# Performance work log

Hardware: AMD Instinct MI355X
Metric: run time of the kernel (lower is better)

The kernel has to match this reference:

```python
import jax, jax.numpy as jnp
import numpy as np

BETA = 1.0  # softmax_beta


def setup_inputs() -> dict:
    key = jax.random.key(0)
    ks = jax.random.split(key, 8)
    B, S, D, K, V, H, O = 32, 513, 1024, 256, 256, 2048, 256
    return {
        "x": jax.random.normal(ks[0], (B, S, D), dtype=jnp.float32),
        "W_Q": jax.random.normal(ks[1], (K, D), dtype=jnp.float32) / (K ** 0.5),
        "W_K": jax.random.normal(ks[2], (K, D), dtype=jnp.float32) / (K ** 0.5),
        "W_V": jax.random.uniform(ks[3], (V, D), dtype=jnp.float32) * 0.1,
        "W_proj": jax.random.normal(ks[4], (O, V), dtype=jnp.float32) / (V ** 0.5),
        "W_hi0": jax.random.uniform(ks[5], (B, H, K), dtype=jnp.float32) * 0.5,
        "W_oh0": jax.random.uniform(ks[6], (B, V, H), dtype=jnp.float32),
        "W_reinst0": jax.random.uniform(ks[7], (B, H, D), dtype=jnp.float32),
    }


def _mhn_forward(x, W_Q, W_K, W_V, W_proj, W_hi0, W_oh0, W_reinst0):
    ctx = x[:, :-1, :]                       # (B, T, D) context one-hot/inputs
    xK = ctx @ W_K.T                          # (B, T, K) items
    xV = ctx @ W_V.T                          # (B, T, V) labels
    xQ = x[:, -1, :] @ W_Q.T                  # (B, K) query
    H = W_hi0.shape[1]

    def step(carry, inp):
        W_hi, W_oh, W_reinst = carry
        xk, xv, c = inp                       # (B,K), (B,V), (B,D)
        logits = jnp.einsum("bhk,bk->bh", W_hi, xk)
        # top-1 winner-take-all (sparsify_tensor with k=1 along hidden dim)
        z = jax.nn.one_hot(jnp.argmax(logits, axis=1), H, dtype=W_hi.dtype)  # (B,H)
        # winner row/column replaced by current item / label / context
        W_reinst = W_reinst + z[:, :, None] * (c[:, None, :] - W_reinst)
        W_hi = W_hi + z[:, :, None] * (xk[:, None, :] - W_hi)
        W_oh = W_oh + z[:, None, :] * (xv[:, :, None] - W_oh)
        return (W_hi, W_oh, W_reinst), None

    xs = (xK.transpose(1, 0, 2), xV.transpose(1, 0, 2), ctx.transpose(1, 0, 2))
    (W_hi, W_oh, W_reinst), _ = jax.lax.scan(step, (W_hi0, W_oh0, W_reinst0), xs)

    # query / readout step
    h = jax.nn.softmax(BETA * jnp.einsum("bhk,bk->bh", W_hi, xQ), axis=1)
    mhn_out = jnp.einsum("bvh,bh->bv", W_oh, h)          # (B, V)
    reinst_context = jnp.einsum("bhd,bh->bd", W_reinst, h)  # (B, D)
    out = mhn_out @ W_proj.T                              # (B, O)
    return out, reinst_context, xQ


def reference(x, W_Q, W_K, W_V, W_proj, W_hi0, W_oh0, W_reinst0):
    return _mhn_forward(x, W_Q, W_K, W_V, W_proj, W_hi0, W_oh0, W_reinst0)
```

## Files before the change

### kernel.cpp

```cpp
#include <hip/hip_runtime.h>
#include <math.h>

#define BB 32
#define SFULL 513
#define TT 512
#define DD 1024
#define KK 256
#define VV 256
#define HH 2048
#define OO 256

template <typename AT, typename BT, typename CT>
__global__ __launch_bounds__(256) void gemm_abt(
    const AT* __restrict__ A, long long aBatch, int aPitch,
    const BT* __restrict__ Bm, long long bBatch, int bPitch,
    CT* __restrict__ C, long long cBatch, int cPitch, int Kd) {
  const int bz = blockIdx.z;
  A  += (size_t)bz * aBatch;
  Bm += (size_t)bz * bBatch;
  C  += (size_t)bz * cBatch;
  const int m0 = blockIdx.y * 64;
  const int n0 = blockIdx.x * 64;
  const int tid = threadIdx.x;
  const int tx = tid & 15;
  const int ty = tid >> 4;
  const int rl = tid >> 2;
  const int kq = tid & 3;

  __shared__ AT As[16][65];
  __shared__ BT Bs[16][65];

  CT acc[4][4];
#pragma unroll
  for (int i = 0; i < 4; i++)
#pragma unroll
    for (int j = 0; j < 4; j++) acc[i][j] = (CT)0;

  for (int kk = 0; kk < Kd; kk += 16) {
    const AT* ap = A + (size_t)(m0 + rl) * aPitch + kk + kq * 4;
    const BT* bp = Bm + (size_t)(n0 + rl) * bPitch + kk + kq * 4;
#pragma unroll
    for (int i = 0; i < 4; i++) As[kq * 4 + i][rl] = ap[i];
#pragma unroll
    for (int i = 0; i < 4; i++) Bs[kq * 4 + i][rl] = bp[i];
    __syncthreads();
#pragma unroll
    for (int k = 0; k < 16; k++) {
      CT a[4], b[4];
#pragma unroll
      for (int i = 0; i < 4; i++) a[i] = (CT)As[k][ty * 4 + i];
#pragma unroll
      for (int j = 0; j < 4; j++) b[j] = (CT)Bs[k][tx * 4 + j];
#pragma unroll
      for (int i = 0; i < 4; i++)
#pragma unroll
        for (int j = 0; j < 4; j++) acc[i][j] += a[i] * b[j];
    }
    __syncthreads();
  }

#pragma unroll
  for (int i = 0; i < 4; i++) {
    CT* cp = C + (size_t)(m0 + ty * 4 + i) * cPitch + n0 + tx * 4;
#pragma unroll
    for (int j = 0; j < 4; j++) cp[j] = acc[i][j];
  }
}

__global__ __launch_bounds__(256) void xq_kernel(const float* __restrict__ x,
                                                 const float* __restrict__ W_Q,
                                                 float* __restrict__ xQws,
                                                 float* __restrict__ outp) {
  const int b = blockIdx.x;
  const int tid = threadIdx.x;
  const int w = tid >> 6, lane = tid & 63;
  const float* xr = x + ((size_t)b * SFULL + TT) * DD;
  for (int n = w; n < KK; n += 4) {
    const float* wq = W_Q + (size_t)n * DD;
    float s = 0.f;
    for (int k = lane; k < DD; k += 64) s += wq[k] * xr[k];
#pragma unroll
    for (int off = 32; off; off >>= 1) s += __shfl_down(s, off);
    if (lane == 0) {
      xQws[b * KK + n] = s;
      outp[BB * OO + BB * DD + b * KK + n] = s;
    }
  }
}

#define SCAN_STEP(T, CUR, PI0, PI1, PIG, PO0, PO1, POG)                       \
  {                                                                           \
         \
    int rn = (T) + 2;                                                         \
    if (rn > TT - 1) rn = TT - 1;                                             \
    const double* lr = L0b + (size_t)rn * HH;                                 \
    PO0 = lr[tid];                                                            \
    PO1 = lr[tid + 1024];                                                     \
    const double* gr = Gb + (size_t)rn * TT;                                  \
    POG = (tid < TT) ? gr[tid] : 0.0;                                         \
                                      \
    int l1 = last[tid];                                                       \
    int l2 = last[tid + 1024];                                                \
    int g1 = l1 < 0 ? 0 : l1;                                                 \
    int g2 = l2 < 0 ? 0 : l2;                                                 \
    double v1 = (l1 < 0) ? Lb[CUR][tid] : Gr[CUR][g1];                        \
    double v2 = (l2 < 0) ? Lb[CUR][tid + 1024] : Gr[CUR][g2];                 \
    double v;                                                                 \
    int idx;                                                                  \
    if (v2 > v1) { v = v2; idx = tid + 1024; }                                \
    else { v = v1; idx = tid; }                     \
    _Pragma("unroll")                                                         \
    for (int off = 32; off; off >>= 1) {                                      \
      double ov = __shfl_down(v, off);                                        \
      int oi = __shfl_down(idx, off);                                         \
      if (ov > v || (ov == v && oi < idx)) { v = ov; idx = oi; }              \
    }                                                                         \
    if ((tid & 63) == 0) { rv[tid >> 6] = v; ri[tid >> 6] = idx; }            \
    asm volatile("s_waitcnt lgkmcnt(0)" ::: "memory");                        \
    __builtin_amdgcn_s_barrier();                              \
    if (tid < 64) {                                                           \
      double vv = (tid < 16) ? rv[tid] : -INFINITY;                           \
      int ii = (tid < 16) ? ri[tid] : 0x7fffffff;                             \
      _Pragma("unroll")                                                       \
      for (int off = 8; off; off >>= 1) {                                     \
        double ov = __shfl_down(vv, off);                                     \
        int oi = __shfl_down(ii, off);                                        \
        if (ov > vv || (ov == vv && oi < ii)) { vv = ov; ii = oi; }           \
      }                                                                       \
      if (tid == 0) last[ii] = (T);                                           \
    }                                                                         \
               \
    Lb[(CUR) ^ 1][tid] = PI0;                                                 \
    Lb[(CUR) ^ 1][tid + 1024] = PI1;                                          \
    if (tid < TT) Gr[(CUR) ^ 1][tid] = PIG;                                   \
    asm volatile("s_waitcnt lgkmcnt(0)" ::: "memory");                        \
    __builtin_amdgcn_s_barrier();                              \
  }

__global__ __launch_bounds__(1024) void scan_kernel(const double* __restrict__ L0t,
                                                    const double* __restrict__ Gram,
                                                    int* __restrict__ lastmap) {
  const int b = blockIdx.x;
  const int tid = threadIdx.x;
  __shared__ double Lb[2][HH];
  __shared__ double Gr[2][TT];
  __shared__ int last[HH];
  __shared__ double rv[16];
  __shared__ int ri[16];

  const double* L0b = L0t + (size_t)b * TT * HH;
  const double* Gb = Gram + (size_t)b * TT * TT;

  last[tid] = -1;
  last[tid + 1024] = -1;

  double pA0, pA1, pAg;
  double pB0, pB1, pBg;

  double r00 = L0b[tid];
  double r01 = L0b[tid + 1024];
  pB0 = L0b[HH + tid];
  pB1 = L0b[HH + tid + 1024];
  pBg = (tid < TT) ? Gb[TT + tid] : 0.0;
  Lb[0][tid] = r00;
  Lb[0][tid + 1024] = r01;
  asm volatile("s_waitcnt lgkmcnt(0)" ::: "memory");
  __builtin_amdgcn_s_barrier();

  for (int t = 0; t < TT; t += 2) {
    SCAN_STEP(t,     0, pB0, pB1, pBg, pA0, pA1, pAg);
    SCAN_STEP(t + 1, 1, pA0, pA1, pAg, pB0, pB1, pBg);
  }

  lastmap[b * HH + tid] = last[tid];
  lastmap[b * HH + tid + 1024] = last[tid + 1024];
}

__global__ __launch_bounds__(1024) void epi1_kernel(const float* __restrict__ W_hi0,
                                                    const double* __restrict__ xK64,
                                                    const float* __restrict__ xQws,
                                                    const int* __restrict__ lastmap,
                                                    float* __restrict__ hvmg,
                                                    float* __restrict__ wgtg) {
  const int b = blockIdx.x;
  const int tid = threadIdx.x;
  const int w = tid >> 6, lane = tid & 63;
  __shared__ float xq[KK];
  __shared__ float ql[HH];
  __shared__ float red[16];
  __shared__ float redsum[16];
  if (tid < KK) xq[tid] = xQws[b * KK + tid];
  if (tid < TT) wgtg[b * TT + tid] = 0.f;
  __syncthreads();

  for (int h = w; h < HH; h += 16) {
    int li = lastmap[b * HH + h];
    float s = 0.f;
    if (li < 0) {
      const float* p = W_hi0 + ((size_t)b * HH + h) * KK;
      for (int k = lane; k < KK; k += 64) s += p[k] * xq[k];
    } else {
      const double* p = xK64 + ((size_t)b * TT + li) * KK;
      for (int k = lane; k < KK; k += 64) s += (float)p[k] * xq[k];
    }
#pragma unroll
    for (int off = 32; off; off >>= 1) s += __shfl_down(s, off);
    if (lane == 0) ql[h] = s;
  }
  __syncthreads();

  float lm = fmaxf(ql[tid], ql[tid + 1024]);
#pragma unroll
  for (int off = 32; off; off >>= 1) lm = fmaxf(lm, __shfl_down(lm, off));
  if (lane == 0) red[w] = lm;
  __syncthreads();
  if (tid == 0) {
    float m = red[0];
    for (int i = 1; i < 16; i++) m = fmaxf(m, red[i]);
    red[0] = m;
  }
  __syncthreads();
  const float mx = red[0];
  float e1 = expf(ql[tid] - mx);
  float e2 = expf(ql[tid + 1024] - mx);
  float ls = e1 + e2;
#pragma unroll
  for (int off = 32; off; off >>= 1) ls += __shfl_down(ls, off);
  if (lane == 0) redsum[w] = ls;
  __syncthreads();
  if (tid == 0) {
    float s = 0.f;
    for (int i = 0; i < 16; i++) s += redsum[i];
    redsum[0] = s;
  }
  __syncthreads();
  const float inv = 1.f / redsum[0];
  const float hv1 = e1 * inv, hv2 = e2 * inv;
  const int li1 = lastmap[b * HH + tid];
  const int li2 = lastmap[b * HH + tid + 1024];
  hvmg[b * HH + tid] = (li1 < 0) ? hv1 : 0.f;
  hvmg[b * HH + tid + 1024] = (li2 < 0) ? hv2 : 0.f;
  if (li1 >= 0) wgtg[b * TT + li1] = hv1;
  if (li2 >= 0) wgtg[b * TT + li2] = hv2;
}

#define RCH 20

__global__ __launch_bounds__(256) void epi2_partial(const float* __restrict__ W_reinst0,
                                                    const float* __restrict__ x,
                                                    const float* __restrict__ hvmg,
                                                    const float* __restrict__ wgtg,
                                                    float* __restrict__ partial) {
  const int c = blockIdx.x;
  const int b = blockIdx.y;
  const int tid = threadIdx.x;
  const int r0 = c * 128;
  __shared__ float wsh[128];
  if (tid < 128) {
    const int gr = r0 + tid;
    wsh[tid] = (gr < HH) ? hvmg[b * HH + gr] : wgtg[b * TT + (gr - HH)];
  }
  __syncthreads();
  const int d = tid * 4;
  float4 acc = make_float4(0.f, 0.f, 0.f, 0.f);
#pragma unroll 4
  for (int r = 0; r < 128; r++) {
    const float wv = wsh[r];
    if (wv == 0.f) continue;
    const int gr = r0 + r;
    const float* src = (gr < HH)
        ? W_reinst0 + ((size_t)b * HH + gr) * DD
        : x + ((size_t)b * SFULL + (gr - HH)) * DD;
    const float4 v = *reinterpret_cast<const float4*>(src + d);
    acc.x += wv * v.x;
    acc.y += wv * v.y;
    acc.z += wv * v.z;
    acc.w += wv * v.w;
  }
  *reinterpret_cast<float4*>(partial + ((size_t)b * RCH + c) * DD + d) = acc;
}

__global__ __launch_bounds__(256) void epi2_reduce(const float* __restrict__ partial,
                                                   float* __restrict__ outp) {
  const int b = blockIdx.x;
  const int d = threadIdx.x * 4;
  float4 acc = make_float4(0.f, 0.f, 0.f, 0.f);
#pragma unroll
  for (int c = 0; c < RCH; c++) {
    const float4 v = *reinterpret_cast<const float4*>(partial + ((size_t)b * RCH + c) * DD + d);
    acc.x += v.x;
    acc.y += v.y;
    acc.z += v.z;
    acc.w += v.w;
  }
  *reinterpret_cast<float4*>(outp + BB * OO + b * DD + d) = acc;
}

__global__ __launch_bounds__(1024) void epi3_kernel(const float* __restrict__ W_oh0,
                                                    const float* __restrict__ xVws,
                                                    const float* __restrict__ W_proj,
                                                    const float* __restrict__ hvmg,
                                                    const float* __restrict__ wgtg,
                                                    float* __restrict__ outp) {
  const int b = blockIdx.x;
  const int tid = threadIdx.x;
  const int w = tid >> 6, lane = tid & 63;
  __shared__ float hvm[HH];
  __shared__ float wgt[TT];
  __shared__ float mhn[VV];
  for (int i = tid; i < HH; i += 1024) hvm[i] = hvmg[b * HH + i];
  if (tid < TT) wgt[tid] = wgtg[b * TT + tid];
  __syncthreads();

  for (int v = w; v < VV; v += 16) {
    const float* p = W_oh0 + ((size_t)b * VV + v) * HH;
    float s = 0.f;
    for (int h = lane; h < HH; h += 64) s += hvm[h] * p[h];
#pragma unroll
    for (int off = 32; off; off >>= 1) s += __shfl_down(s, off);
    if (lane == 0) mhn[v] = s;
  }
  __syncthreads();
  if (tid < VV) {
    float s2 = 0.f;
#pragma unroll 4
    for (int s = 0; s < TT; s++) {
      float wv = wgt[s];
      if (wv != 0.f) s2 += wv * xVws[((size_t)b * TT + s) * VV + tid];
    }
    mhn[tid] += s2;
  }
  __syncthreads();
  for (int o = w; o < OO; o += 16) {
    const float* p = W_proj + (size_t)o * VV;
    float s = 0.f;
    for (int v = lane; v < VV; v += 64) s += mhn[v] * p[v];
#pragma unroll
    for (int off = 32; off; off >>= 1) s += __shfl_down(s, off);
    if (lane == 0) outp[b * OO + o] = s;
  }
}

extern "C" void kernel_launch(void* const* d_in, const int* in_sizes, int n_in,
                              void* d_out, int out_size, void* d_ws, size_t ws_size,
                              hipStream_t stream) {
  const float* x        = (const float*)d_in[0];
  const float* W_Q      = (const float*)d_in[1];
  const float* W_K      = (const float*)d_in[2];
  const float* W_V      = (const float*)d_in[3];
  const float* W_proj   = (const float*)d_in[4];
  const float* W_hi0    = (const float*)d_in[5];
  const float* W_oh0    = (const float*)d_in[6];
  const float* W_reinst0 = (const float*)d_in[7];
  float* outp = (float*)d_out;

  char* ws = (char*)d_ws;
  double* xK64 = (double*)ws;
  double* Gram = (double*)(ws + 33554432);
  double* L0t  = (double*)(ws + 100663296);
  float*  xVws = (float*)(ws + 369098752);
  float*  xQws = (float*)(ws + 385875968);
  int*    lastmap = (int*)(ws + 385908736);
  float*  hvmg = (float*)(ws + 386170880);
  float*  wgtg = (float*)(ws + 386433024);
  float*  partial = (float*)(ws + 33554432);
  (void)ws_size; (void)in_sizes; (void)n_in; (void)out_size;

  gemm_abt<float, float, double><<<dim3(KK / 64, TT / 64, BB), 256, 0, stream>>>(
      x, (long long)SFULL * DD, DD,
      W_K, 0LL, DD,
      xK64, (long long)TT * KK, KK, DD);

  gemm_abt<float, float, float><<<dim3(VV / 64, TT / 64, BB), 256, 0, stream>>>(
      x, (long long)SFULL * DD, DD,
      W_V, 0LL, DD,
      xVws, (long long)TT * VV, VV, DD);

  xq_kernel<<<BB, 256, 0, stream>>>(x, W_Q, xQws, outp);

  gemm_abt<double, float, double><<<dim3(HH / 64, TT / 64, BB), 256, 0, stream>>>(
      xK64, (long long)TT * KK, KK,
      W_hi0, (long long)HH * KK, KK,
      L0t, (long long)TT * HH, HH, KK);

  gemm_abt<double, double, double><<<dim3(TT / 64, TT / 64, BB), 256, 0, stream>>>(
      xK64, (long long)TT * KK, KK,
      xK64, (long long)TT * KK, KK,
      Gram, (long long)TT * TT, TT, KK);

  scan_kernel<<<BB, 1024, 0, stream>>>(L0t, Gram, lastmap);

  epi1_kernel<<<BB, 1024, 0, stream>>>(W_hi0, xK64, xQws, lastmap, hvmg, wgtg);

  epi2_partial<<<dim3(RCH, BB), 256, 0, stream>>>(W_reinst0, x, hvmg, wgtg, partial);
  epi2_reduce<<<BB, 256, 0, stream>>>(partial, outp);

  epi3_kernel<<<BB, 1024, 0, stream>>>(W_oh0, xVws, W_proj, hvmg, wgtg, outp);
}
```

Baseline: 3.397 ms.

## Restructure scan kernel to 256 threads with register-resident state and one barrier per step

The sequential winner-take-all scan now runs with 256 threads per batch, each owning 8 hidden units whose last-write indices and prefetched L0 logits sit in registers instead of shared memory. The argmax uses xor-butterfly shuffles so every wave holds the result, and a single barrier per step replaces two; all threads redundantly reduce the four wave partials. This targets barrier and LDS latency on the serial 512-step critical path. The cost is more registers per thread and more serial per-thread work, with only 32 blocks active.

```diff
diff --git a/kernel.cpp b/kernel.cpp
--- a/kernel.cpp
+++ b/kernel.cpp
@@ -88,92 +88,121 @@
   }
 }
 
-#define SCAN_STEP(T, CUR, PI0, PI1, PIG, PO0, PO1, POG)                       \
+#define STEP(T, CUR)                                                          \
   {                                                                           \
+    double bv;                                                                \
+    int bh;                                                                   \
+    {                                                                         \
+      double cand[4][2];                                                      \
+      _Pragma("unroll")                                                       \
+      for (int i = 0; i < 4; i++)                                             \
+        _Pragma("unroll")                                                     \
+        for (int j = 0; j < 2; j++) {                                         \
+          int li = last[i][j];                                                \
+          int s0 = li < 0 ? 0 : li;                                           \
+          double gv = gbuf[CUR][s0];                                          \
+          cand[i][j] = li < 0 ? l0[CUR][i][j] : gv;                           \
+        }                                                                     \
+      bv = cand[0][0];                                                        \
+      bh = tid * 2;                                                           \
+      _Pragma("unroll")                                                       \
+      for (int i = 0; i < 4; i++)                                             \
+        _Pragma("unroll")                                                     \
+        for (int j = 0; j < 2; j++) {                                         \
+          if (i == 0 && j == 0) continue;                                     \
+          int h = i * 512 + tid * 2 + j;                                      \
+          double c = cand[i][j];                                              \
+          if (c > bv || (c == bv && h < bh)) { bv = c; bh = h; }              \
+        }                                                                     \
+    }                                                                         \
+                    \
+    _Pragma("unroll")                                                         \
+    for (int m = 1; m < 64; m <<= 1) {                                        \
+      double ov = __shfl_xor(bv, m);                                          \
+      int oh = __shfl_xor(bh, m);                                             \
+      if (ov > bv || (ov == bv && oh < bh)) { bv = ov; bh = oh; }             \
+    }                                                                         \
+    if (lane == 0) { sv[(T) & 1][w] = bv; sh[(T) & 1][w] = bh; }              \
          \
-    int rn = (T) + 2;                                                         \
-    if (rn > TT - 1) rn = TT - 1;                                             \
-    const double* lr = L0b + (size_t)rn * HH;                                 \
-    PO0 = lr[tid];                                                            \
-    PO1 = lr[tid + 1024];                                                     \
-    const double* gr = Gb + (size_t)rn * TT;                                  \
-    POG = (tid < TT) ? gr[tid] : 0.0;                                         \
-                                      \
-    int l1 = last[tid];                                                       \
-    int l2 = last[tid + 1024];                                                \
-    int g1 = l1 < 0 ? 0 : l1;                                                 \
-    int g2 = l2 < 0 ? 0 : l2;                                                 \
-    double v1 = (l1 < 0) ? Lb[CUR][tid] : Gr[CUR][g1];                        \
-    double v2 = (l2 < 0) ? Lb[CUR][tid + 1024] : Gr[CUR][g2];                 \
-    double v;                                                                 \
-    int idx;                                                                  \
-    if (v2 > v1) { v = v2; idx = tid + 1024; }                                \
-    else { v = v1; idx = tid; }                     \
+    {                                                                         \
+      int rn = (T) + 2;                                                       \
+      if (rn > TT - 1) rn = TT - 1;                                           \
+      const double* lp = L0b + (size_t)rn * HH + 2 * tid;                     \
+      _Pragma("unroll")                                                       \
+      for (int i = 0; i < 4; i++) {                                           \
+        l0[CUR][i][0] = lp[i * 512];                                          \
+        l0[CUR][i][1] = lp[i * 512 + 1];                                      \
+      }                                                                       \
+      const double* gp = Gb + (size_t)rn * TT + 2 * tid;                      \
+      double t0 = gpre[(CUR) ^ 1][0], t1 = gpre[(CUR) ^ 1][1];                \
+      gpre[CUR][0] = gp[0];                                                   \
+      gpre[CUR][1] = gp[1];                                                   \
+      gbuf[(CUR) ^ 1][2 * tid] = t0;                                          \
+      gbuf[(CUR) ^ 1][2 * tid + 1] = t1;                                      \
+    }                                                                         \
+    asm volatile("s_waitcnt lgkmcnt(0)" ::: "memory");                        \
+    __builtin_amdgcn_sched_barrier(0);                                        \
+    __builtin_amdgcn_s_barrier();                                             \
+                        \
+    bv = sv[(T) & 1][0];                                                      \
+    bh = sh[(T) & 1][0];                                                      \
     _Pragma("unroll")                                                         \
-    for (int off = 32; off; off >>= 1) {                                      \
-      double ov = __shfl_down(v, off);                                        \
-      int oi = __shfl_down(idx, off);                                         \
-      if (ov > v || (ov == v && oi < idx)) { v = ov; idx = oi; }              \
+    for (int q = 1; q < 4; q++) {                                             \
+      double qv = sv[(T) & 1][q];                                             \
+      int qh = sh[(T) & 1][q];                                                \
+      if (qv > bv || (qv == bv && qh < bh)) { bv = qv; bh = qh; }             \
     }                                                                         \
-    if ((tid & 63) == 0) { rv[tid >> 6] = v; ri[tid >> 6] = idx; }            \
-    asm volatile("s_waitcnt lgkmcnt(0)" ::: "memory");                        \
-    __builtin_amdgcn_s_barrier();                              \
-    if (tid < 64) {                                                           \
-      double vv = (tid < 16) ? rv[tid] : -INFINITY;                           \
-      int ii = (tid < 16) ? ri[tid] : 0x7fffffff;                             \
+                                 \
+    _Pragma("unroll")                                                         \
+    for (int i = 0; i < 4; i++)                                               \
       _Pragma("unroll")                                                       \
-      for (int off = 8; off; off >>= 1) {                                     \
-        double ov = __shfl_down(vv, off);                                     \
-        int oi = __shfl_down(ii, off);                                        \
-        if (ov > vv || (ov == vv && oi < ii)) { vv = ov; ii = oi; }           \
-      }                                                                       \
-      if (tid == 0) last[ii] = (T);                                           \
-    }                                                                         \
-               \
-    Lb[(CUR) ^ 1][tid] = PI0;                                                 \
-    Lb[(CUR) ^ 1][tid + 1024] = PI1;                                          \
-    if (tid < TT) Gr[(CUR) ^ 1][tid] = PIG;                                   \
-    asm volatile("s_waitcnt lgkmcnt(0)" ::: "memory");                        \
-    __builtin_amdgcn_s_barrier();                              \
-  }
-
-__global__ __launch_bounds__(1024) void scan_kernel(const double* __restrict__ L0t,
-                                                    const double* __restrict__ Gram,
-                                                    int* __restrict__ lastmap) {
+      for (int j = 0; j < 2; j++)                                             \
+        if (bh == i * 512 + tid * 2 + j) last[i][j] = (T);                    \
+  }
+
+__global__ __launch_bounds__(256) void scan_kernel(const double* __restrict__ L0t,
+                                                   const double* __restrict__ Gram,
+                                                   int* __restrict__ lastmap) {
   const int b = blockIdx.x;
   const int tid = threadIdx.x;
-  __shared__ double Lb[2][HH];
-  __shared__ double Gr[2][TT];
-  __shared__ int last[HH];
-  __shared__ double rv[16];
-  __shared__ int ri[16];
+  const int lane = tid & 63;
+  const int w = tid >> 6;
+  __shared__ double gbuf[2][TT];
+  __shared__ double sv[2][4];
+  __shared__ int sh[2][4];
 
   const double* L0b = L0t + (size_t)b * TT * HH;
   const double* Gb = Gram + (size_t)b * TT * TT;
 
-  last[tid] = -1;
-  last[tid + 1024] = -1;
-
-  double pA0, pA1, pAg;
-  double pB0, pB1, pBg;
-
-  double r00 = L0b[tid];
-  double r01 = L0b[tid + 1024];
-  pB0 = L0b[HH + tid];
-  pB1 = L0b[HH + tid + 1024];
-  pBg = (tid < TT) ? Gb[TT + tid] : 0.0;
-  Lb[0][tid] = r00;
-  Lb[0][tid + 1024] = r01;
-  asm volatile("s_waitcnt lgkmcnt(0)" ::: "memory");
-  __builtin_amdgcn_s_barrier();
+  int last[4][2];
+  double l0[2][4][2];
+  double gpre[2][2];
+
+#pragma unroll
+  for (int i = 0; i < 4; i++) { last[i][0] = -1; last[i][1] = -1; }
+
+#pragma unroll
+  for (int i = 0; i < 4; i++) {
+    const double* p0 = L0b + (size_t)i * 512 + 2 * tid;
+    l0[0][i][0] = p0[0];
+    l0[0][i][1] = p0[1];
+    const double* p1 = L0b + (size_t)HH + (size_t)i * 512 + 2 * tid;
+    l0[1][i][0] = p1[0];
+    l0[1][i][1] = p1[1];
+  }
+  gpre[1][0] = Gb[TT + 2 * tid];
+  gpre[1][1] = Gb[TT + 2 * tid + 1];
 
   for (int t = 0; t < TT; t += 2) {
-    SCAN_STEP(t,     0, pB0, pB1, pBg, pA0, pA1, pAg);
-    SCAN_STEP(t + 1, 1, pA0, pA1, pAg, pB0, pB1, pBg);
-  }
-
-  lastmap[b * HH + tid] = last[tid];
-  lastmap[b * HH + tid + 1024] = last[tid + 1024];
+    STEP(t, 0);
+    STEP(t + 1, 1);
+  }
+
+#pragma unroll
+  for (int i = 0; i < 4; i++)
+#pragma unroll
+    for (int j = 0; j < 2; j++)
+      lastmap[b * HH + i * 512 + tid * 2 + j] = last[i][j];
 }
 
 __global__ __launch_bounds__(1024) void epi1_kernel(const float* __restrict__ W_hi0,
@@ -388,7 +417,7 @@
       xK64, (long long)TT * KK, KK,
       Gram, (long long)TT * TT, TT, KK);
 
-  scan_kernel<<<BB, 1024, 0, stream>>>(L0t, Gram, lastmap);
+  scan_kernel<<<BB, 256, 0, stream>>>(L0t, Gram, lastmap);
 
   epi1_kernel<<<BB, 1024, 0, stream>>>(W_hi0, xK64, xQws, lastmap, hvmg, wgtg);
 
```

Result: no change. 3.331 ms (-1.9%).
